# Kernel tuning notes

Hardware: AMD Instinct MI355X
Metric: run time of the kernel (lower is better)

The kernel has to match this reference:

```python
import jax, jax.numpy as jnp
import numpy as np
from math import factorial

# ---- module hyperparameters (from init_kwargs) ----
SPECIES = np.array([1, 6, 7, 8], np.int32)
LOW, HIGH, NG, RSWITCH, W, LMAX = 0.0, 6.0, 20, 1.0, 2.0, 2
LWEIGHTS = np.array([1.0, 1.0, 1.0], np.float32)
INVF = [2.0, 2.0, 2.0]


def _angular_tables():
    comps, weights, idx, inv = [], [], [], []
    for i in range(LMAX + 1):
        for k in range(i + 1):
            for m in range(i - k + 1):
                n = i - k - m
                comps.append([n, m, k])
                weights.append(factorial(i) / (factorial(n) * factorial(m) * factorial(k)))
                idx.append(i)
                inv.append(INVF[i])
    return (np.array(comps, np.int32), np.array(weights, np.float32),
            np.array(idx, np.int32), np.array(inv, np.float32))

COMPS, ANGW, ANGIDX, INVFACT = _angular_tables()   # 10 angular components for lmax=2
OFFSETS = np.linspace(LOW, HIGH, NG + 1, dtype=np.float32)[1:]
SQRTPI = np.float32(np.sqrt(np.pi))
NSP = len(SPECIES)
COMBOS = [(i, j) for i in range(NSP) for j in range(i + 1, NSP)]
NMBODY = NSP + len(COMBOS)
FPSIZE = NG * (LMAX + 1) * NMBODY


def _int_pow(x, e):
    # e in {0,1,2}; avoids NaN from pow(negative_base, float_exponent)
    return jnp.where(e == 0, jnp.ones_like(x), jnp.where(e == 1, x, x * x))


def _forward(coordinates, nuclear_charges, natom_counts, neighbours):
    B, N, _ = coordinates.shape
    mask = neighbours >= 0                              # padded slots are -1
    nb = jnp.maximum(neighbours, 0)                     # safe_fill
    bidx = jnp.arange(B)[:, None, None]
    local = coordinates[bidx, nb]                       # [B,N,M,3] neighbour gather
    nbh = coordinates[:, :, None, :] - local
    nbh = jnp.where(mask[..., None], nbh, 1.0)          # keep padded slots finite
    d = jnp.linalg.norm(nbh, axis=3)                    # [B,N,M]
    coeff = mask.astype(coordinates.dtype)
    nbr_z = nuclear_charges[bidx, nb]                   # [B,N,M]

    dsw = (d - RSWITCH) / (HIGH - RSWITCH)
    cut = 1.0 - 6.0 * dsw**5 + 15.0 * dsw**4 - 10.0 * dsw**3
    d2 = d * d
    sigma2 = jnp.log(1.0 + W / d2)
    mu = jnp.log(d / jnp.sqrt(1.0 + W / d2))
    off = jnp.asarray(OFFSETS)
    centered = (jnp.log(off) - mu[..., None]) ** 2      # [B,N,M,G]
    s2 = sigma2[..., None]
    radial = (1.0 / (off * jnp.sqrt(s2) * SQRTPI)) * jnp.exp(-centered / (2.0 * s2)) \
             * cut[..., None] * coeff[..., None]        # [B,N,M,G]

    expo = jnp.asarray(INVFACT + ANGIDX.astype(np.float32))
    inv_scaling = (1.0 / d[..., None]) ** expo * coeff[..., None]   # [B,N,M,A]
    comps = jnp.asarray(COMPS)
    angular = inv_scaling \
        * _int_pow(nbh[..., None, 0], comps[:, 0]) \
        * _int_pow(nbh[..., None, 1], comps[:, 1]) \
        * _int_pow(nbh[..., None, 2], comps[:, 2])      # [B,N,M,A]

    angw = jnp.asarray(ANGW)
    lw = jnp.asarray(LWEIGHTS)
    onehot = jnp.asarray((ANGIDX[:, None] == np.arange(LMAX + 1)[None, :]).astype(np.float32))

    sp_masks = [(nbr_z == int(z)).astype(coordinates.dtype) for z in SPECIES]

    def group_fp(gmask):
        ang = angular * gmask[..., None]
        t = jnp.einsum('bnma,bnmg->bnag', ang, radial)          # sum over neighbours
        orb = angw[None, None, :, None] * (t * t)               # [B,N,A,G]
        elem = jnp.einsum('bnag,al->bnlg', orb, onehot)         # index_add over l
        return lw[None, None, :, None] * elem                   # [B,N,L+1,G]

    fps = [group_fp(m) for m in sp_masks]
    for (i, j) in COMBOS:
        gmask = jnp.maximum(sp_masks[i], sp_masks[j])
        fps.append(group_fp(gmask) - (fps[i] + fps[j]))

    fp = jnp.stack(fps, axis=3)                                 # [B,N,L+1,NMBODY,G]
    atom_mask = (jnp.arange(N)[None, :] < natom_counts[:, None]).astype(coordinates.dtype)
    fp = fp * atom_mask[:, :, None, None, None]
    return fp.reshape(B, N, FPSIZE)


def setup_inputs() -> dict:
    rng = np.random.default_rng(0)
    B, N, M = 128, 128, 64
    box = 13.5
    coords = rng.uniform(0.0, box, (B, N, 3)).astype(np.float32)
    charges = rng.choice(np.array([1, 6, 7, 8], np.int32), size=(B, N)).astype(np.int32)
    counts = rng.integers(96, N + 1, B).astype(np.int32)
    diff = coords[:, :, None, :] - coords[:, None, :, :]
    dist = np.linalg.norm(diff, axis=-1)
    exist = np.arange(N)[None, :] < counts[:, None]
    valid = (dist < HIGH) & (dist > 1e-6) & exist[:, :, None] & exist[:, None, :]
    order = np.argsort(~valid, axis=2, kind='stable')[:, :, :M]
    vmask = np.take_along_axis(valid, order, axis=2)
    neighbours = np.where(vmask, order, -1).astype(np.int32)
    return {
        "coordinates": jnp.asarray(coords),
        "nuclear_charges": jnp.asarray(charges),
        "natom_counts": jnp.asarray(counts),
        "neighbours": jnp.asarray(neighbours),
    }


def reference(coordinates, nuclear_charges, natom_counts, neighbours):
    return _forward(coordinates, nuclear_charges, natom_counts, neighbours)
```

## Files before the change

kernel.cpp:

```cpp
#include <hip/hip_runtime.h>


#define B_   128
#define N_   128
#define M_   64
#define NG_  20
#define NSP_ 4
#define FPSIZE_ 600
#define APB  16
#define NTASK (APB * M_)
#define BLOCK_THREADS (APB * NG_)

__global__ __launch_bounds__(BLOCK_THREADS)
void gto_fp_kernel(const float* __restrict__ coords,
                   const int*   __restrict__ charges,
                   const int*   __restrict__ counts,
                   const int*   __restrict__ neigh,
                   float*       __restrict__ out)
{
    __shared__ float4 sA[APB][M_];
    __shared__ float2 sB[APB][M_];
    __shared__ int s_cnt[APB][NSP_];
    __shared__ int s_start[APB][NSP_];
    __shared__ int s_pos[APB][NSP_];

    const int tid = threadIdx.x;
    const int blockBase = blockIdx.x * APB;
    const int bidx = blockBase / N_;

    if (tid < APB * NSP_) ((int*)s_cnt)[tid] = 0;
    __syncthreads();

    float4 rA[4]; float2 rB[4]; int rls[4]; int nrec = 0;
    for (int t = tid; t < NTASK; t += BLOCK_THREADS) {
        const int la = t >> 6;
        const int m  = t & 63;
        const int atom = blockBase + la;
        const int nb = neigh[atom * M_ + m];
        if (nb < 0) continue;
        const int nidx = bidx * N_ + nb;
        const float dx = coords[atom * 3 + 0] - coords[nidx * 3 + 0];
        const float dy = coords[atom * 3 + 1] - coords[nidx * 3 + 1];
        const float dz = coords[atom * 3 + 2] - coords[nidx * 3 + 2];
        const int   z  = charges[nidx];

        const float d2     = dx * dx + dy * dy + dz * dz;
        const float inv_d  = __builtin_amdgcn_rsqf(d2);
        const float d      = d2 * inv_d;
        const float inv_d2 = inv_d * inv_d;
        const float ux = dx * inv_d, uy = dy * inv_d, uz = dz * inv_d;

        const float dsw  = (d - 1.0f) * 0.2f;
        const float dsw2 = dsw * dsw;
        const float cut  = 1.0f - dsw2 * dsw * fmaf(6.0f, dsw2, fmaf(-15.0f, dsw, 10.0f));

        const float sigma2 = __logf(fmaf(2.0f, inv_d2, 1.0f));
        const float mu     = 0.5f * (__logf(d2) - sigma2);
        const float fold   = -0.72134752f * __builtin_amdgcn_rcpf(sigma2);
        const float amp    = __builtin_amdgcn_rsqf(sigma2) * cut * inv_d2;

        const int s = (z == 1) ? 0 : (z - 5);
        atomicAdd(&s_cnt[la][s], 1);
        rA[nrec] = make_float4(ux, uy, uz, mu);
        rB[nrec] = make_float2(fold, amp);
        rls[nrec] = (la << 2) | s;
        ++nrec;
    }
    __syncthreads();

    if (tid < APB) {
        const int c0 = s_cnt[tid][0], c1 = s_cnt[tid][1], c2 = s_cnt[tid][2];
        s_start[tid][0] = 0;            s_pos[tid][0] = 0;
        s_start[tid][1] = c0;           s_pos[tid][1] = c0;
        s_start[tid][2] = c0 + c1;      s_pos[tid][2] = c0 + c1;
        s_start[tid][3] = c0 + c1 + c2; s_pos[tid][3] = c0 + c1 + c2;
    }
    __syncthreads();

    for (int r = 0; r < nrec; ++r) {
        const int la = rls[r] >> 2, s = rls[r] & 3;
        const int slot = atomicAdd(&s_pos[la][s], 1);
        sA[la][slot] = rA[r];
        sB[la][slot] = rB[r];
    }
    __syncthreads();

    const int g  = tid % NG_;
    const int la = tid / NG_;
    const int atom = blockBase + la;
    const int n = atom % N_;

    const float off         = 0.3f * (float)(g + 1);
    const float log_off     = __logf(off);
    const float inv_off_spi = 1.0f / (off * 1.7724538509055159f);

    float T[NSP_][10];
#pragma unroll
    for (int s = 0; s < NSP_; ++s)
#pragma unroll
        for (int a = 0; a < 10; ++a) T[s][a] = 0.0f;

#define ACC(SS)                                                               \
    {                                                                         \
        const int e0 = s_start[la][SS];                                       \
        const int e1 = e0 + s_cnt[la][SS];                                    \
        for (int m = e0; m < e1; ++m) {                                       \
            const float4 A  = sA[la][m];                                      \
            const float2 Bv = sB[la][m];                                      \
            const float cen = log_off - A.w;                                  \
            const float ex  = __builtin_amdgcn_exp2f(Bv.x * cen * cen);       \
            const float rad = Bv.y * ex;                                      \
            const float rx = rad * A.x, ry = rad * A.y, rz = rad * A.z;       \
            T[SS][0] += rad;                                                  \
            T[SS][1] += rx;  T[SS][2] += ry;  T[SS][3] += rz;                 \
            T[SS][4] = fmaf(rx, A.x, T[SS][4]);                               \
            T[SS][5] = fmaf(rx, A.y, T[SS][5]);                               \
            T[SS][6] = fmaf(ry, A.y, T[SS][6]);                               \
            T[SS][7] = fmaf(rx, A.z, T[SS][7]);                               \
            T[SS][8] = fmaf(ry, A.z, T[SS][8]);                               \
            T[SS][9] = fmaf(rz, A.z, T[SS][9]);                               \
        }                                                                     \
    }
    ACC(0) ACC(1) ACC(2) ACC(3)
#undef ACC

    const float amask = (n < counts[bidx]) ? 1.0f : 0.0f;
    const float scale = amask * inv_off_spi * inv_off_spi;
    float* op = out + atom * FPSIZE_ + g;

#pragma unroll
    for (int l = 0; l < 3; ++l) {
        const int a0 = (l == 0) ? 0 : (l == 1) ? 1 : 4;
        const int a1 = (l == 0) ? 1 : (l == 1) ? 4 : 10;
#pragma unroll
        for (int s = 0; s < NSP_; ++s) {
            float v = 0.0f;
#pragma unroll
            for (int a = a0; a < a1; ++a) {
                const float w = (a == 5 || a == 7 || a == 8) ? 2.0f : 1.0f;
                v = fmaf(w * T[s][a], T[s][a], v);
            }
            op[(l * 10 + s) * NG_] = scale * v;
        }
        int mb = 4;
#pragma unroll
        for (int i = 0; i < NSP_; ++i) {
#pragma unroll
            for (int j = i + 1; j < NSP_; ++j) {
                float v = 0.0f;
#pragma unroll
                for (int a = a0; a < a1; ++a) {
                    const float w = (a == 5 || a == 7 || a == 8) ? 2.0f : 1.0f;
                    v = fmaf(w * T[i][a], T[j][a], v);
                }
                op[(l * 10 + mb) * NG_] = scale * (2.0f * v);
                ++mb;
            }
        }
    }
}

extern "C" void kernel_launch(void* const* d_in, const int* in_sizes, int n_in,
                              void* d_out, int out_size, void* d_ws, size_t ws_size,
                              hipStream_t stream) {
    const float* coords  = (const float*)d_in[0];
    const int*   charges = (const int*)d_in[1];
    const int*   counts  = (const int*)d_in[2];
    const int*   neigh   = (const int*)d_in[3];
    float*       outp    = (float*)d_out;

    const int blocks = (B_ * N_) / APB;
    gto_fp_kernel<<<blocks, BLOCK_THREADS, 0, stream>>>(coords, charges, counts, neigh, outp);
}
```

Measured before the change: 94.12 us.

## Fold radial Gaussian into single exp2 polynomial with half-packed records

Expands the squared log-distance term so each neighbour's radial factor becomes exp2 of a quadratic in log(offset), folding the amplitude in through a log2 term. Coefficients and unit vectors are packed as fp16 pairs into one float4 per neighbour, removing the separate float2 array. The species histogram is now built in a separate pre-pass, so records go straight to shared memory instead of being held in registers. The inner loop is unrolled by two and the shared array gets one padding element per row. The fp16 coefficients (especially the quadratic and linear ones) may lose accuracy, and the neighbour and charge loads are now done twice.

```diff
diff --git a/kernel.cpp b/kernel.cpp
--- a/kernel.cpp
+++ b/kernel.cpp
@@ -1,4 +1,5 @@
 #include <hip/hip_runtime.h>
+#include <hip/hip_fp16.h>
 
 
 #define B_   128
@@ -18,8 +19,7 @@
                    const int*   __restrict__ neigh,
                    float*       __restrict__ out)
 {
-    __shared__ float4 sA[APB][M_];
-    __shared__ float2 sB[APB][M_];
+    __shared__ float4 sR[APB][M_ + 1];
     __shared__ int s_cnt[APB][NSP_];
     __shared__ int s_start[APB][NSP_];
     __shared__ int s_pos[APB][NSP_];
@@ -31,10 +31,28 @@
     if (tid < APB * NSP_) ((int*)s_cnt)[tid] = 0;
     __syncthreads();
 
-    float4 rA[4]; float2 rB[4]; int rls[4]; int nrec = 0;
     for (int t = tid; t < NTASK; t += BLOCK_THREADS) {
-        const int la = t >> 6;
-        const int m  = t & 63;
+        const int la = t >> 6, m = t & 63;
+        const int nb = neigh[(blockBase + la) * M_ + m];
+        if (nb >= 0) {
+            const int z = charges[bidx * N_ + nb];
+            const int s = (z == 1) ? 0 : (z - 5);
+            atomicAdd(&s_cnt[la][s], 1);
+        }
+    }
+    __syncthreads();
+
+    if (tid < APB) {
+        const int c0 = s_cnt[tid][0], c1 = s_cnt[tid][1], c2 = s_cnt[tid][2];
+        s_start[tid][0] = 0;            s_pos[tid][0] = 0;
+        s_start[tid][1] = c0;           s_pos[tid][1] = c0;
+        s_start[tid][2] = c0 + c1;      s_pos[tid][2] = c0 + c1;
+        s_start[tid][3] = c0 + c1 + c2; s_pos[tid][3] = c0 + c1 + c2;
+    }
+    __syncthreads();
+
+    for (int t = tid; t < NTASK; t += BLOCK_THREADS) {
+        const int la = t >> 6, m = t & 63;
         const int atom = blockBase + la;
         const int nb = neigh[atom * M_ + m];
         if (nb < 0) continue;
@@ -48,7 +66,6 @@
         const float inv_d  = __builtin_amdgcn_rsqf(d2);
         const float d      = d2 * inv_d;
         const float inv_d2 = inv_d * inv_d;
-        const float ux = dx * inv_d, uy = dy * inv_d, uz = dz * inv_d;
 
         const float dsw  = (d - 1.0f) * 0.2f;
         const float dsw2 = dsw * dsw;
@@ -56,32 +73,26 @@
 
         const float sigma2 = __logf(fmaf(2.0f, inv_d2, 1.0f));
         const float mu     = 0.5f * (__logf(d2) - sigma2);
-        const float fold   = -0.72134752f * __builtin_amdgcn_rcpf(sigma2);
-        const float amp    = __builtin_amdgcn_rsqf(sigma2) * cut * inv_d2;
+        const float amp    = fmaxf(__builtin_amdgcn_rsqf(sigma2) * cut * inv_d2,
+                                   1.0e-30f);
+
+        const float F   = -0.72134752f * __builtin_amdgcn_rcpf(sigma2);
+        const float Fm  = F * mu;
+        const float c1v = -(Fm + Fm);
+        const float c2v = fmaf(Fm, mu, __log2f(amp));
+
+        const __half2 hc = __floats2half2_rn(F, c1v);
+        const __half2 hu = __floats2half2_rn(dx * inv_d, dy * inv_d);
+        const __half2 hw = __floats2half2_rn(dz * inv_d, 0.0f);
+        float4 rec;
+        rec.x = *(const float*)&hc;
+        rec.y = c2v;
+        rec.z = *(const float*)&hu;
+        rec.w = *(const float*)&hw;
 
         const int s = (z == 1) ? 0 : (z - 5);
-        atomicAdd(&s_cnt[la][s], 1);
-        rA[nrec] = make_float4(ux, uy, uz, mu);
-        rB[nrec] = make_float2(fold, amp);
-        rls[nrec] = (la << 2) | s;
-        ++nrec;
-    }
-    __syncthreads();
-
-    if (tid < APB) {
-        const int c0 = s_cnt[tid][0], c1 = s_cnt[tid][1], c2 = s_cnt[tid][2];
-        s_start[tid][0] = 0;            s_pos[tid][0] = 0;
-        s_start[tid][1] = c0;           s_pos[tid][1] = c0;
-        s_start[tid][2] = c0 + c1;      s_pos[tid][2] = c0 + c1;
-        s_start[tid][3] = c0 + c1 + c2; s_pos[tid][3] = c0 + c1 + c2;
-    }
-    __syncthreads();
-
-    for (int r = 0; r < nrec; ++r) {
-        const int la = rls[r] >> 2, s = rls[r] & 3;
         const int slot = atomicAdd(&s_pos[la][s], 1);
-        sA[la][slot] = rA[r];
-        sB[la][slot] = rB[r];
+        sR[la][slot] = rec;
     }
     __syncthreads();
 
@@ -90,8 +101,9 @@
     const int atom = blockBase + la;
     const int n = atom % N_;
 
-    const float off         = 0.3f * (float)(g + 1);
-    const float log_off     = __logf(off);
+    const float off = 0.3f * (float)(g + 1);
+    const float lo  = __logf(off);
+    const float lo2 = lo * lo;
     const float inv_off_spi = 1.0f / (off * 1.7724538509055159f);
 
     float T[NSP_][10];
@@ -99,30 +111,47 @@
     for (int s = 0; s < NSP_; ++s)
 #pragma unroll
         for (int a = 0; a < 10; ++a) T[s][a] = 0.0f;
+
+#define BODY(SS, R)                                                           \
+    {                                                                         \
+        const __half2 hc = *(const __half2*)&R.x;                             \
+        const __half2 hu = *(const __half2*)&R.z;                             \
+        const __half2 hw = *(const __half2*)&R.w;                             \
+        const float c0 = __low2float(hc), c1 = __high2float(hc);              \
+        const float ux = __low2float(hu), uy = __high2float(hu);              \
+        const float uz = __low2float(hw);                                     \
+        const float rad = __builtin_amdgcn_exp2f(                             \
+            fmaf(c0, lo2, fmaf(c1, lo, R.y)));                                \
+        const float rx = rad * ux, ry = rad * uy, rz = rad * uz;              \
+        T[SS][0] += rad;                                                      \
+        T[SS][1] += rx;  T[SS][2] += ry;  T[SS][3] += rz;                     \
+        T[SS][4] = fmaf(rx, ux, T[SS][4]);                                    \
+        T[SS][5] = fmaf(rx, uy, T[SS][5]);                                    \
+        T[SS][6] = fmaf(ry, uy, T[SS][6]);                                    \
+        T[SS][7] = fmaf(rx, uz, T[SS][7]);                                    \
+        T[SS][8] = fmaf(ry, uz, T[SS][8]);                                    \
+        T[SS][9] = fmaf(rz, uz, T[SS][9]);                                    \
+    }
 
 #define ACC(SS)                                                               \
     {                                                                         \
         const int e0 = s_start[la][SS];                                       \
         const int e1 = e0 + s_cnt[la][SS];                                    \
-        for (int m = e0; m < e1; ++m) {                                       \
-            const float4 A  = sA[la][m];                                      \
-            const float2 Bv = sB[la][m];                                      \
-            const float cen = log_off - A.w;                                  \
-            const float ex  = __builtin_amdgcn_exp2f(Bv.x * cen * cen);       \
-            const float rad = Bv.y * ex;                                      \
-            const float rx = rad * A.x, ry = rad * A.y, rz = rad * A.z;       \
-            T[SS][0] += rad;                                                  \
-            T[SS][1] += rx;  T[SS][2] += ry;  T[SS][3] += rz;                 \
-            T[SS][4] = fmaf(rx, A.x, T[SS][4]);                               \
-            T[SS][5] = fmaf(rx, A.y, T[SS][5]);                               \
-            T[SS][6] = fmaf(ry, A.y, T[SS][6]);                               \
-            T[SS][7] = fmaf(rx, A.z, T[SS][7]);                               \
-            T[SS][8] = fmaf(ry, A.z, T[SS][8]);                               \
-            T[SS][9] = fmaf(rz, A.z, T[SS][9]);                               \
+        int m = e0;                                                           \
+        for (; m + 1 < e1; m += 2) {                                          \
+            const float4 Ra = sR[la][m];                                      \
+            const float4 Rb = sR[la][m + 1];                                  \
+            BODY(SS, Ra)                                                      \
+            BODY(SS, Rb)                                                      \
+        }                                                                     \
+        if (m < e1) {                                                         \
+            const float4 Ra = sR[la][m];                                      \
+            BODY(SS, Ra)                                                      \
         }                                                                     \
     }
     ACC(0) ACC(1) ACC(2) ACC(3)
 #undef ACC
+#undef BODY
 
     const float amask = (n < counts[bidx]) ? 1.0f : 0.0f;
     const float scale = amask * inv_off_spi * inv_off_spi;
```

Measured after the change: 86.50 us. 8.1% less time.
